# Kernel optimization log

Hardware: AMD Instinct MI355X
Metric: run time of the kernel (lower is better)

The kernel has to match this reference:

```python
import jax, jax.numpy as jnp
import numpy as np
from jax import lax

B, S, T = 256, 128, 64
IN, MID, HID = 4, 128, 512
NH = 4  # attention heads


def setup_inputs() -> dict:
    key = jax.random.key(0)
    ks = iter(jax.random.split(key, 64))
    def p(*shape):
        return jax.random.normal(next(ks), shape, jnp.float32) * 0.05
    d = {}
    d["src"] = jax.random.normal(next(ks), (B, S, IN), jnp.float32)
    d["trg"] = jax.random.normal(next(ks), (B, T, IN), jnp.float32)
    # fc_in: IN -> MID//4 -> MID//2 -> MID
    d["fi_w1"] = p(MID // 4, IN); d["fi_b1"] = p(MID // 4)
    d["fi_w2"] = p(MID // 2, MID // 4); d["fi_b2"] = p(MID // 2)
    d["fi_w3"] = p(MID, MID // 2); d["fi_b3"] = p(MID)
    # encoder: 2-layer bidirectional LSTM (layer0 in=MID, layer1 in=2*HID)
    for name, ind in [("e0", MID), ("e1", 2 * HID)]:
        for sfx in ["f", "b"]:
            d[name + sfx + "_wih"] = p(4 * HID, ind)
            d[name + sfx + "_whh"] = p(4 * HID, HID)
            d[name + sfx + "_bih"] = p(4 * HID)
            d[name + sfx + "_bhh"] = p(4 * HID)
    d["attnfc_w"] = p(MID, 2 * HID); d["attnfc_b"] = p(MID)
    d["inproj_w"] = p(3 * MID, MID); d["inproj_b"] = p(3 * MID)
    d["outproj_w"] = p(MID, MID); d["outproj_b"] = p(MID)
    # decoder: 2-layer unidirectional LSTM (layer0 in=MID, layer1 in=HID)
    for name, ind in [("d0", MID), ("d1", HID)]:
        d[name + "_wih"] = p(4 * HID, ind)
        d[name + "_whh"] = p(4 * HID, HID)
        d[name + "_bih"] = p(4 * HID)
        d[name + "_bhh"] = p(4 * HID)
    # fc_out: HID -> MID//2 -> MID//4 -> IN
    d["fo_w1"] = p(MID // 2, HID); d["fo_b1"] = p(MID // 2)
    d["fo_w2"] = p(MID // 4, MID // 2); d["fo_b2"] = p(MID // 4)
    d["fo_w3"] = p(IN, MID // 4); d["fo_b3"] = p(IN)
    return d


def _gelu(x):
    return jax.nn.gelu(x, approximate=False)  # torch default GELU is exact


def _mlp3(x, w1, b1, w2, b2, w3, b3):
    h = _gelu(x @ w1.T + b1)
    h = _gelu(h @ w2.T + b2)
    return h @ w3.T + b3


def _lstm(x, h0, c0, wih, whh, bih, bhh, reverse=False):
    """PyTorch-semantics LSTM layer. x: (B,T,in) -> (hs (B,T,H), h_T, c_T)."""
    xg = jnp.einsum('bti,gi->btg', x, wih) + (bih + bhh)  # fold input GEMM over time
    def step(carry, xt):
        h, c = carry
        g = xt + h @ whh.T
        i, f, gg, o = jnp.split(g, 4, axis=-1)  # torch gate order: i,f,g,o
        c = jax.nn.sigmoid(f) * c + jax.nn.sigmoid(i) * jnp.tanh(gg)
        h = jax.nn.sigmoid(o) * jnp.tanh(c)
        return (h, c), h
    (h, c), hs = lax.scan(step, (h0, c0), jnp.swapaxes(xg, 0, 1), reverse=reverse)
    return jnp.swapaxes(hs, 0, 1), h, c


def _mha(q_in, kv, inproj_w, inproj_b, outproj_w, outproj_b):
    E = q_in.shape[-1]
    dh = E // NH
    wq, wk, wv = jnp.split(inproj_w, 3, axis=0)
    bq, bk, bv = jnp.split(inproj_b, 3)
    q = q_in @ wq.T + bq
    k = kv @ wk.T + bk
    v = kv @ wv.T + bv
    hd = lambda x: x.reshape(x.shape[0], x.shape[1], NH, dh)
    scores = jnp.einsum('bqhd,bkhd->bhqk', hd(q), hd(k)) * (1.0 / float(np.sqrt(dh)))
    a = jax.nn.softmax(scores, axis=-1)
    o = jnp.einsum('bhqk,bkhd->bqhd', a, hd(v)).reshape(q.shape)
    return o @ outproj_w.T + outproj_b


def reference(src, trg,
              fi_w1, fi_b1, fi_w2, fi_b2, fi_w3, fi_b3,
              e0f_wih, e0f_whh, e0f_bih, e0f_bhh, e0b_wih, e0b_whh, e0b_bih, e0b_bhh,
              e1f_wih, e1f_whh, e1f_bih, e1f_bhh, e1b_wih, e1b_whh, e1b_bih, e1b_bhh,
              attnfc_w, attnfc_b, inproj_w, inproj_b, outproj_w, outproj_b,
              d0_wih, d0_whh, d0_bih, d0_bhh, d1_wih, d1_whh, d1_bih, d1_bhh,
              fo_w1, fo_b1, fo_w2, fo_b2, fo_w3, fo_b3):
    bsz = src.shape[0]
    z = jnp.zeros((bsz, HID), src.dtype)
    enc_embed = _mlp3(src, fi_w1, fi_b1, fi_w2, fi_b2, fi_w3, fi_b3)
    # encoder layer 0 (bidirectional)
    l0f, hf0, cf0 = _lstm(enc_embed, z, z, e0f_wih, e0f_whh, e0f_bih, e0f_bhh)
    l0b, hb0, cb0 = _lstm(enc_embed, z, z, e0b_wih, e0b_whh, e0b_bih, e0b_bhh, reverse=True)
    x1 = jnp.concatenate([l0f, l0b], axis=-1)
    # encoder layer 1 (bidirectional)
    l1f, hf1, cf1 = _lstm(x1, z, z, e1f_wih, e1f_whh, e1f_bih, e1f_bhh)
    l1b, hb1, cb1 = _lstm(x1, z, z, e1b_wih, e1b_whh, e1b_bih, e1b_bhh, reverse=True)
    enc_out = jnp.concatenate([l1f, l1b], axis=-1)  # (B,S,2H)
    # h.view(L,2,B,H).sum(dim=1): sum forward+backward final states per layer
    h_l0, c_l0 = hf0 + hb0, cf0 + cb0
    h_l1, c_l1 = hf1 + hb1, cf1 + cb1
    proj_enc = jnp.tanh(enc_out @ attnfc_w.T + attnfc_b)  # (B,S,MID)
    # teacher_forcing_ratio = 1.0 -> decoder inputs are exactly trg[:, 0:T]
    inp = _mlp3(trg, fi_w1, fi_b1, fi_w2, fi_b2, fi_w3, fi_b3)  # (B,T,MID)
    attn_out = _mha(inp, proj_enc, inproj_w, inproj_b, outproj_w, outproj_b)
    dec_input = inp + attn_out
    d0, _, _ = _lstm(dec_input, h_l0, c_l0, d0_wih, d0_whh, d0_bih, d0_bhh)
    d1, _, _ = _lstm(d0, h_l1, c_l1, d1_wih, d1_whh, d1_bih, d1_bhh)
    delta = _mlp3(d1, fo_w1, fo_b1, fo_w2, fo_b2, fo_w3, fo_b3)
    return trg + delta  # pred_t = trg[:, t-1] + delta_t
```

## Files before the change

### kernel.cpp

```cpp
#include <hip/hip_runtime.h>
#include <cstdint>
#include <cstddef>
#include <cstdio>

typedef __bf16 bf16;
typedef __bf16 bf16x8 __attribute__((ext_vector_type(8)));
typedef __bf16 bf16x4 __attribute__((ext_vector_type(4)));
typedef float f32x4 __attribute__((ext_vector_type(4)));

#define DEVFN __device__ __forceinline__

DEVFN float geluf(float x) { return 0.5f * x * (1.0f + erff(x * 0.70710678118654752f)); }
DEVFN float sigmoidf(float x) { return 1.0f / (1.0f + expf(-x)); }

template <int WGM, int WGN, int ACT, bool RES>
__launch_bounds__(WGM * WGN * 64)
__global__ void gemm_bt(const bf16* __restrict__ A, const bf16* __restrict__ W,
                        const float* __restrict__ bias, const bf16* __restrict__ Rsd,
                        bf16* __restrict__ C, int M, int N, int K) {
  constexpr int BM = WGM * 64, BN = WGN * 64, T = WGM * WGN * 64;
  constexpr int NA = BM * 4 / T, NB = BN * 4 / T;
  __shared__ __align__(16) char ldsA[BM * 64];
  __shared__ __align__(16) char ldsB[BN * 64];
  const int tid = threadIdx.x;
// ... 130 lines not shown
                              int M, int N, int K) {
  constexpr int WGM = 2, WGN = 1;
  constexpr int BM = WGM * 64, BN = WGN * 64, T = WGM * WGN * 64;
  constexpr int NA = BM * 4 / T, NB = BN * 4 / T;
  __shared__ __align__(16) char ldsA[BM * 64];
  __shared__ __align__(16) char ldsB[BN * 64];
  const int tid = threadIdx.x;
  const int lane = tid & 63, wave = tid >> 6;
  const int wm = wave % WGM, wn = wave / WGM;
  const int l16 = lane & 15, quad = lane >> 4;
  const int bm0 = blockIdx.x * BM, bn0 = blockIdx.y * BN;

  f32x4 acc[4][4] = {};
  for (int k0 = 0; k0 < K; k0 += 32) {
    bf16x8 ta[NA], tb[NB];
#pragma unroll
    for (int i = 0; i < NA; ++i) {
      int lin = i * T + tid;
      int row = bm0 + (lin >> 2), seg = lin & 3;
      int t = row >> 8, b = row & 255;
      ta[i] = *(const bf16x8*)(HC + (size_t)t * 131072 + (size_t)((k0 >> 3) + seg) * 2048 + b * 8);
    }
#pragma unroll
    for (int i = 0; i < NB; ++i) {
      int lin = i * T + tid;
      int row = lin >> 2, seg = lin & 3;
      tb[i] = *(const bf16x8*)(W + (size_t)(bn0 + row) * K + k0 + seg * 8);
    }
#pragma unroll
    for (int i = 0; i < NA; ++i) *(bf16x8*)(ldsA + (i * T + tid) * 16) = ta[i];
#pragma unroll
    for (int i = 0; i < NB; ++i) *(bf16x8*)(ldsB + (i * T + tid) * 16) = tb[i];
    __syncthreads();
    bf16x8 af[4], bfrag[4];
#pragma unroll
    for (int mi = 0; mi < 4; ++mi)
      af[mi] = *(const bf16x8*)(ldsA + (wm * 64 + mi * 16 + l16) * 64 + quad * 16);
#pragma unroll
    for (int ni = 0; ni < 4; ++ni)
      bfrag[ni] = *(const bf16x8*)(ldsB + (wn * 64 + ni * 16 + l16) * 64 + quad * 16);
#pragma unroll
    for (int mi = 0; mi < 4; ++mi)
#pragma unroll
      for (int ni = 0; ni < 4; ++ni)
        acc[mi][ni] = __builtin_amdgcn_mfma_f32_16x16x32_bf16(af[mi], bfrag[ni], acc[mi][ni], 0, 0, 0);
    __syncthreads();
  }
#pragma unroll
  for (int mi = 0; mi < 4; ++mi) {
#pragma unroll
    for (int ni = 0; ni < 4; ++ni) {
      int col = bn0 + wn * 64 + ni * 16 + l16;
      float bv = bias[col];
#pragma unroll
      for (int r = 0; r < 4; ++r) {
        int row = bm0 + wm * 64 + mi * 16 + quad * 4 + r;
        float x = geluf(acc[mi][ni][r] + bv);
        C[(size_t)row * N + col] = (bf16)x;
      }
    }
  }
}

template <int HCMODE>
DEVFN void xg_tile(const bf16* __restrict__ A, int tbase, const bf16* __restrict__ W,
                   const float* __restrict__ bias, bf16* __restrict__ C,
                   int K, int bm0, int bn0, int tid, bf16* ldsA, bf16* ldsB) {
  const int lane = tid & 63, wave = tid >> 6;
  const int wm = wave & 1, wn = wave >> 1;
  const int l16 = lane & 15, quad = lane >> 4;
  f32x4 acc[4][4] = {};
  for (int k0 = 0; k0 < K; k0 += 32) {
    bf16x8 ta, tb0, tb1;
    {
      int row = bm0 + (tid >> 2), seg = tid & 3;
      if (HCMODE) {
        int t = tbase + (row >> 8), b = row & 255;
        ta = *(const bf16x8*)(A + (size_t)t * 262144 + (size_t)((k0 >> 3) + seg) * 2048 + b * 8);
      } else {
        ta = *(const bf16x8*)(A + (size_t)row * K + k0 + seg * 8);
      }
    }
    { int row = tid >> 2, seg = tid & 3;
      tb0 = *(const bf16x8*)(W + (size_t)(bn0 + row) * K + k0 + seg * 8); }
    { int lin = 512 + tid; int row = lin >> 2, seg = lin & 3;
      tb1 = *(const bf16x8*)(W + (size_t)(bn0 + row) * K + k0 + seg * 8); }
    *(bf16x8*)(ldsA + tid * 8) = ta;
    *(bf16x8*)(ldsB + tid * 8) = tb0;
    *(bf16x8*)(ldsB + (512 + tid) * 8) = tb1;
    __syncthreads();
    bf16x8 af[4], bfr[4];
#pragma unroll
    for (int mi = 0; mi < 4; ++mi)
      af[mi] = *(const bf16x8*)(ldsA + (wm * 64 + mi * 16 + l16) * 32 + quad * 8);
#pragma unroll
    for (int ni = 0; ni < 4; ++ni)
      bfr[ni] = *(const bf16x8*)(ldsB + (wn * 64 + ni * 16 + l16) * 32 + quad * 8);
#pragma unroll
    for (int mi = 0; mi < 4; ++mi)
#pragma unroll
      for (int ni = 0; ni < 4; ++ni)
        acc[mi][ni] = __builtin_amdgcn_mfma_f32_16x16x32_bf16(af[mi], bfr[ni], acc[mi][ni], 0, 0, 0);
    __syncthreads();
  }
#pragma unroll
  for (int mi = 0; mi < 4; ++mi) {
#pragma unroll
    for (int ni = 0; ni < 4; ++ni) {
      int col = bn0 + wn * 64 + ni * 16 + l16;
      float bv = bias[col];
#pragma unroll
      for (int r = 0; r < 4; ++r) {
        int row = bm0 + wm * 64 + mi * 16 + quad * 4 + r;
        C[(size_t)row * 2048 + col] = (bf16)(acc[mi][ni][r] + bv);
      }
    }
  }
}

struct RDir {
  const bf16* whh_r;
  const bf16* xg;
  bf16* hc;
  int slcOff, rev;
  const bf16* h0;
  float* cbuf;
  bf16* hfin;
};

struct GJob {
  int mode;
  const bf16* Af; const bf16* Ab;
  int tbF, tbB;
  const bf16* Wf; const bf16* Wb;
  const float* bsF; const float* bsB;
  bf16* outF; bf16* outB;
};

__launch_bounds__(512, 1)
__global__ void lstm_rec_g(RDir da, RDir db, int t0, int tc, int Tfull,
                           int* __restrict__ cnts, GJob job) {
  __shared__ __align__(16) char smem[36864];
  const int blk = blockIdx.x;
  const int tid = threadIdx.x;

  if (blk >= 128) {
    if (job.mode == 0) return;
    bf16* ldsA = (bf16*)smem;
    bf16* ldsB = (bf16*)(smem + 8192);
    const int gb = blk - 128;
    const int K = (job.mode == 2) ? 1024 : 128;
    for (int tile = gb; tile < 512; tile += 128) {
      int dir = tile >> 8;
      int rem = tile & 255;
      int mi = rem >> 3, ni = rem & 7;
      const bf16* A = dir ? job.Ab : job.Af;
      int tb = dir ? job.tbB : job.tbF;
      const bf16* W = dir ? job.Wb : job.Wf;
      const float* bs = dir ? job.bsB : job.bsF;
      bf16* C = dir ? job.outB : job.outF;
      if (job.mode == 2)
        xg_tile<1>(A, tb, W, bs, C, K, mi * 128, ni * 256, tid, ldsA, ldsB);
      else
        xg_tile<0>(A, tb, W, bs, C, K, mi * 128, ni * 256, tid, ldsA, ldsB);
    }
    return;
  }

  bf16* whh_lds = (bf16*)smem;
  bf16* hstg = (bf16*)(smem + 32768);
  const RDir d = (blk >= 64) ? db : da;
  const int slice = blk & 63;
  const int colBase = slice * 32, unitBase = slice * 8;
  const int w = tid >> 6, lane = tid & 63;
  const int l16 = lane & 15, quad = lane >> 4;

  for (int e = tid * 8; e < 32 * 512; e += 512 * 8) {
    int c = e >> 9, k0 = e & 511;
    bf16x8 v = *(const bf16x8*)(d.whh_r + (size_t)(colBase + c) * 512 + k0);
    *(bf16x8*)(whh_lds + ((k0 >> 3) << 8) + (c << 3)) = v;
  }
  float cst[2][2];
#pragma unroll
  for (int m = 0; m < 2; ++m)
#pragma unroll
    for (int i = 0; i < 2; ++i) {
      int b = (w * 2 + i) * 16 + l16;
      cst[m][i] = d.cbuf[(size_t)b * 512 + unitBase + m * 4 + quad];
    }
  __syncthreads();

  int* cnt = cnts + (blk & 64);
  const int b0 = (w * 2) * 16 + l16;
  const int b1 = b0 + 16;

  for (int s = 0; s < tc; ++s) {
    const int sg = t0 + s;
    const int t = d.rev ? (Tfull - 1 - sg) : sg;
    const int lt = d.rev ? (tc - 1 - s) : s;

    bf16x4 gxr[2][2];
#pragma unroll
    for (int m = 0; m < 2; ++m)
#pragma unroll
      for (int i = 0; i < 2; ++i) {
        int b = b0 + i * 16;
        gxr[m][i] = *(const bf16x4*)(d.xg + ((size_t)lt * 256 + b) * 2048 + colBase + m * 16 + quad * 4);
      }
    bf16x8 hr[16][2];
    if (sg == 0) {
      const bf16* hp0 = d.h0 + (size_t)b0 * 512 + quad * 8;
      const bf16* hp1 = d.h0 + (size_t)b1 * 512 + quad * 8;
#pragma unroll
      for (int kk = 0; kk < 16; ++kk) {
        hr[kk][0] = *(const bf16x8*)(hp0 + kk * 32);
        hr[kk][1] = *(const bf16x8*)(hp1 + kk * 32);
      }
    } else {
      const int tp = d.rev ? (t + 1) : (t - 1);
      const bf16* hc = d.hc + (size_t)tp * 262144 + (size_t)d.slcOff * 2048;
#pragma unroll
      for (int kk = 0; kk < 16; ++kk) {
        int u8 = kk * 4 + quad;
        hr[kk][0] = *(const bf16x8*)(hc + u8 * 2048 + (size_t)b0 * 8);
        hr[kk][1] = *(const bf16x8*)(hc + u8 * 2048 + (size_t)b1 * 8);
      }
    }
    __builtin_amdgcn_sched_barrier(0);

    f32x4 acc[2][2] = {};
#pragma unroll
    for (int kk = 0; kk < 16; ++kk) {
      bf16x8 a0 = *(const bf16x8*)(whh_lds + kk * 1024 + quad * 256 + l16 * 8);
      bf16x8 a1 = *(const bf16x8*)(whh_lds + kk * 1024 + quad * 256 + 128 + l16 * 8);
      acc[0][0] = __builtin_amdgcn_mfma_f32_16x16x32_bf16(a0, hr[kk][0], acc[0][0], 0, 0, 0);
      acc[1][0] = __builtin_amdgcn_mfma_f32_16x16x32_bf16(a1, hr[kk][0], acc[1][0], 0, 0, 0);
      acc[0][1] = __builtin_amdgcn_mfma_f32_16x16x32_bf16(a0, hr[kk][1], acc[0][1], 0, 0, 0);
      acc[1][1] = __builtin_amdgcn_mfma_f32_16x16x32_bf16(a1, hr[kk][1], acc[1][1], 0, 0, 0);
    }
#pragma unroll
    for (int m = 0; m < 2; ++m)
#pragma unroll
      for (int i = 0; i < 2; ++i) {
        float gi = acc[m][i][0] + (float)gxr[m][i][0];
        float gf = acc[m][i][1] + (float)gxr[m][i][1];
        float gg = acc[m][i][2] + (float)gxr[m][i][2];
        float go = acc[m][i][3] + (float)gxr[m][i][3];
        float cn = sigmoidf(gf) * cst[m][i] + sigmoidf(gi) * tanhf(gg);
        float hv = sigmoidf(go) * tanhf(cn);
        cst[m][i] = cn;
        int b = (w * 2 + i) * 16 + l16;
        hstg[b * 8 + m * 4 + quad] = (bf16)hv;
      }
    __syncthreads();
    {
      unsigned long long v = *(const unsigned long long*)(hstg + tid * 4);
      __hip_atomic_store((unsigned long long*)(d.hc + (size_t)t * 262144 +
                                               (size_t)(d.slcOff + slice) * 2048 + tid * 4),
                         v, __ATOMIC_RELAXED, __HIP_MEMORY_SCOPE_AGENT);
    }
    __syncthreads();
    if (s < tc - 1 && tid == 0)
      __hip_atomic_fetch_add(cnt, 1, __ATOMIC_RELAXED, __HIP_MEMORY_SCOPE_AGENT);
    if (sg == Tfull - 1 && d.hfin && tid < 256) {
      const unsigned long long* p = (const unsigned long long*)(hstg + tid * 8);
      unsigned long long* r2 = (unsigned long long*)(d.hfin + (size_t)tid * 512 + unitBase);
      r2[0] = p[0]; r2[1] = p[1];
    }
    if (s < tc - 1) {
      if (w == 0) {
        int target = 64 * (s + 1), guard = 0;
        while (__hip_atomic_load(cnt, __ATOMIC_RELAXED, __HIP_MEMORY_SCOPE_AGENT) < target) {
          __builtin_amdgcn_s_sleep(2);
          if (++guard > (1 << 22)) break;
        }
      }
      __syncthreads();
    }
  }
#pragma unroll
  for (int m = 0; m < 2; ++m)
#pragma unroll
    for (int i = 0; i < 2; ++i) {
      int b = (w * 2 + i) * 16 + l16;
      d.cbuf[(size_t)b * 512 + unitBase + m * 4 + quad] = cst[m][i];
    }
}

__launch_bounds__(512, 1)
__global__ void lstm_dec_fused(
    const bf16* __restrict__ whh0, const bf16* __restrict__ xg0,
    bf16* __restrict__ hc0, const bf16* __restrict__ h0d0, float* __restrict__ c0buf,
    const bf16* __restrict__ whh1, const bf16* __restrict__ wih1, const float* __restrict__ bias1,
    bf16* __restrict__ hc1, const bf16* __restrict__ h0d1,
    float* __restrict__ c1buf, int* __restrict__ cnts) {
  const int blk = blockIdx.x;
  const int tid = threadIdx.x;
  const int w = tid >> 6, lane = tid & 63;
  const int l16 = lane & 15, quad = lane >> 4;
  constexpr int TC = 64;

  __shared__ __align__(16) bf16 wldsA[32 * 512];
  __shared__ __align__(16) bf16 wldsB[32 * 512];
  __shared__ __align__(16) bf16 hstg[256 * 8];

  int* cnt0 = cnts;
  int* cnt1 = cnts + 64;
  const int b0 = (w * 2) * 16 + l16;
  const int b1 = b0 + 16;

  if (blk < 64) {
    const int slice = blk;
    const int colBase = slice * 32;
    for (int e = tid * 8; e < 32 * 512; e += 512 * 8) {
      int c = e >> 9, k0 = e & 511;
      bf16x8 v = *(const bf16x8*)(whh0 + (size_t)(colBase + c) * 512 + k0);
      *(bf16x8*)(wldsA + ((k0 >> 3) << 8) + (c << 3)) = v;
    }
    float cst[2][2];
#pragma unroll
    for (int m = 0; m < 2; ++m)
#pragma unroll
      for (int i = 0; i < 2; ++i) {
        int b = (w * 2 + i) * 16 + l16;
        cst[m][i] = c0buf[(size_t)b * 512 + slice * 8 + m * 4 + quad];
      }
    __syncthreads();

    for (int s = 0; s < TC; ++s) {
      bf16x4 gxr[2][2];
#pragma unroll
      for (int m = 0; m < 2; ++m)
#pragma unroll
        for (int i = 0; i < 2; ++i) {
          int b = b0 + i * 16;
          gxr[m][i] = *(const bf16x4*)(xg0 + ((size_t)s * 256 + b) * 2048 + colBase + m * 16 + quad * 4);
        }
      bf16x8 hr[16][2];
      if (s == 0) {
        const bf16* hp0 = h0d0 + (size_t)b0 * 512 + quad * 8;
        const bf16* hp1 = h0d0 + (size_t)b1 * 512 + quad * 8;
#pragma unroll
        for (int kk = 0; kk < 16; ++kk) {
          hr[kk][0] = *(const bf16x8*)(hp0 + kk * 32);
          hr[kk][1] = *(const bf16x8*)(hp1 + kk * 32);
        }
      } else {
        const bf16* hc = hc0 + (size_t)(s - 1) * 131072;
#pragma unroll
        for (int kk = 0; kk < 16; ++kk) {
          int u8 = kk * 4 + quad;
          hr[kk][0] = *(const bf16x8*)(hc + u8 * 2048 + (size_t)b0 * 8);
          hr[kk][1] = *(const bf16x8*)(hc + u8 * 2048 + (size_t)b1 * 8);
        }
      }
      __builtin_amdgcn_sched_barrier(0);
      f32x4 acc[2][2] = {};
#pragma unroll
      for (int kk = 0; kk < 16; ++kk) {
        bf16x8 a0 = *(const bf16x8*)(wldsA + kk * 1024 + quad * 256 + l16 * 8);
        bf16x8 a1 = *(const bf16x8*)(wldsA + kk * 1024 + quad * 256 + 128 + l16 * 8);
        acc[0][0] = __builtin_amdgcn_mfma_f32_16x16x32_bf16(a0, hr[kk][0], acc[0][0], 0, 0, 0);
        acc[1][0] = __builtin_amdgcn_mfma_f32_16x16x32_bf16(a1, hr[kk][0], acc[1][0], 0, 0, 0);
        acc[0][1] = __builtin_amdgcn_mfma_f32_16x16x32_bf16(a0, hr[kk][1], acc[0][1], 0, 0, 0);
        acc[1][1] = __builtin_amdgcn_mfma_f32_16x16x32_bf16(a1, hr[kk][1], acc[1][1], 0, 0, 0);
      }
#pragma unroll
      for (int m = 0; m < 2; ++m)
#pragma unroll
        for (int i = 0; i < 2; ++i) {
          float gi = acc[m][i][0] + (float)gxr[m][i][0];
          float gf = acc[m][i][1] + (float)gxr[m][i][1];
          float gg = acc[m][i][2] + (float)gxr[m][i][2];
          float go = acc[m][i][3] + (float)gxr[m][i][3];
          float cn = sigmoidf(gf) * cst[m][i] + sigmoidf(gi) * tanhf(gg);
          float hv = sigmoidf(go) * tanhf(cn);
          cst[m][i] = cn;
          int b = (w * 2 + i) * 16 + l16;
          hstg[b * 8 + m * 4 + quad] = (bf16)hv;
        }
      __syncthreads();
      {
        unsigned long long v = *(const unsigned long long*)(hstg + tid * 4);
        __hip_atomic_store((unsigned long long*)(hc0 + (size_t)s * 131072 + slice * 2048 + tid * 4),
                           v, __ATOMIC_RELAXED, __HIP_MEMORY_SCOPE_AGENT);
      }
      __syncthreads();
      if (tid == 0)
        __hip_atomic_fetch_add(cnt0, 1, __ATOMIC_RELAXED, __HIP_MEMORY_SCOPE_AGENT);
      if (s < TC - 1) {
        if (w == 0) {
          int target = 64 * (s + 1), guard = 0;
          while (__hip_atomic_load(cnt0, __ATOMIC_RELAXED, __HIP_MEMORY_SCOPE_AGENT) < target) {
            __builtin_amdgcn_s_sleep(2);
            if (++guard > (1 << 22)) break;
          }
        }
        __syncthreads();
      }
    }
#pragma unroll
    for (int m = 0; m < 2; ++m)
#pragma unroll
      for (int i = 0; i < 2; ++i) {
        int b = (w * 2 + i) * 16 + l16;
        c0buf[(size_t)b * 512 + slice * 8 + m * 4 + quad] = cst[m][i];
      }
  } else {
    const int slice = blk - 64;
    const int colBase = slice * 32;
    for (int e = tid * 8; e < 32 * 512; e += 512 * 8) {
      int c = e >> 9, k0 = e & 511;
      bf16x8 v = *(const bf16x8*)(whh1 + (size_t)(colBase + c) * 512 + k0);
      *(bf16x8*)(wldsA + ((k0 >> 3) << 8) + (c << 3)) = v;
      bf16x8 u = *(const bf16x8*)(wih1 + (size_t)(colBase + c) * 512 + k0);
      *(bf16x8*)(wldsB + ((k0 >> 3) << 8) + (c << 3)) = u;
    }
    float gbv[2][4];
#pragma unroll
    for (int m = 0; m < 2; ++m)
#pragma unroll
      for (int r = 0; r < 4; ++r) gbv[m][r] = bias1[colBase + m * 16 + quad * 4 + r];
    float cst[2][2];
#pragma unroll
    for (int m = 0; m < 2; ++m)
#pragma unroll
      for (int i = 0; i < 2; ++i) {
        int b = (w * 2 + i) * 16 + l16;
        cst[m][i] = c1buf[(size_t)b * 512 + slice * 8 + m * 4 + quad];
      }
    __syncthreads();
    if (w == 0) {
      int guard = 0;
      while (__hip_atomic_load(cnt0, __ATOMIC_RELAXED, __HIP_MEMORY_SCOPE_AGENT) < 64) {
        __builtin_amdgcn_s_sleep(2);
        if (++guard > (1 << 22)) break;
      }
    }
    __syncthreads();

    for (int s = 0; s < TC; ++s) {
      f32x4 acc[2][2] = {};
      {
        bf16x8 hr[16][2];
        if (s == 0) {
          const bf16* hp0 = h0d1 + (size_t)b0 * 512 + quad * 8;
          const bf16* hp1 = h0d1 + (size_t)b1 * 512 + quad * 8;
#pragma unroll
          for (int kk = 0; kk < 16; ++kk) {
            hr[kk][0] = *(const bf16x8*)(hp0 + kk * 32);
            hr[kk][1] = *(const bf16x8*)(hp1 + kk * 32);
          }
        } else {
          const bf16* hc = hc1 + (size_t)(s - 1) * 131072;
#pragma unroll
          for (int kk = 0; kk < 16; ++kk) {
            int u8 = kk * 4 + quad;
            hr[kk][0] = *(const bf16x8*)(hc + u8 * 2048 + (size_t)b0 * 8);
            hr[kk][1] = *(const bf16x8*)(hc + u8 * 2048 + (size_t)b1 * 8);
          }
        }
        __builtin_amdgcn_sched_barrier(0);
#pragma unroll
        for (int kk = 0; kk < 16; ++kk) {
          bf16x8 a0 = *(const bf16x8*)(wldsA + kk * 1024 + quad * 256 + l16 * 8);
          bf16x8 a1 = *(const bf16x8*)(wldsA + kk * 1024 + quad * 256 + 128 + l16 * 8);
          acc[0][0] = __builtin_amdgcn_mfma_f32_16x16x32_bf16(a0, hr[kk][0], acc[0][0], 0, 0, 0);
          acc[1][0] = __builtin_amdgcn_mfma_f32_16x16x32_bf16(a1, hr[kk][0], acc[1][0], 0, 0, 0);
          acc[0][1] = __builtin_amdgcn_mfma_f32_16x16x32_bf16(a0, hr[kk][1], acc[0][1], 0, 0, 0);
          acc[1][1] = __builtin_amdgcn_mfma_f32_16x16x32_bf16(a1, hr[kk][1], acc[1][1], 0, 0, 0);
        }
      }
      {
        const bf16* xc = hc0 + (size_t)s * 131072;
        bf16x8 xr[16][2];
#pragma unroll
        for (int kk = 0; kk < 16; ++kk) {
          int u8 = kk * 4 + quad;
          xr[kk][0] = *(const bf16x8*)(xc + u8 * 2048 + (size_t)b0 * 8);
          xr[kk][1] = *(const bf16x8*)(xc + u8 * 2048 + (size_t)b1 * 8);
        }
        __builtin_amdgcn_sched_barrier(0);
#pragma unroll
        for (int kk = 0; kk < 16; ++kk) {
          bf16x8 aw0 = *(const bf16x8*)(wldsB + kk * 1024 + quad * 256 + l16 * 8);
          bf16x8 aw1 = *(const bf16x8*)(wldsB + kk * 1024 + quad * 256 + 128 + l16 * 8);
          acc[0][0] = __builtin_amdgcn_mfma_f32_16x16x32_bf16(aw0, xr[kk][0], acc[0][0], 0, 0, 0);
          acc[1][0] = __builtin_amdgcn_mfma_f32_16x16x32_bf16(aw1, xr[kk][0], acc[1][0], 0, 0, 0);
          acc[0][1] = __builtin_amdgcn_mfma_f32_16x16x32_bf16(aw0, xr[kk][1], acc[0][1], 0, 0, 0);
          acc[1][1] = __builtin_amdgcn_mfma_f32_16x16x32_bf16(aw1, xr[kk][1], acc[1][1], 0, 0, 0);
        }
      }
#pragma unroll
      for (int m = 0; m < 2; ++m)
#pragma unroll
        for (int i = 0; i < 2; ++i) {
          float gi = acc[m][i][0] + gbv[m][0];
          float gf = acc[m][i][1] + gbv[m][1];
          float gg = acc[m][i][2] + gbv[m][2];
          float go = acc[m][i][3] + gbv[m][3];
          float cn = sigmoidf(gf) * cst[m][i] + sigmoidf(gi) * tanhf(gg);
          float hv = sigmoidf(go) * tanhf(cn);
          cst[m][i] = cn;
          int b = (w * 2 + i) * 16 + l16;
          hstg[b * 8 + m * 4 + quad] = (bf16)hv;
        }
      __syncthreads();
      {
        unsigned long long v = *(const unsigned long long*)(hstg + tid * 4);
        __hip_atomic_store((unsigned long long*)(hc1 + (size_t)s * 131072 + slice * 2048 + tid * 4),
                           v, __ATOMIC_RELAXED, __HIP_MEMORY_SCOPE_AGENT);
      }
      __syncthreads();
      if (s < TC - 1) {
        if (tid == 0)
          __hip_atomic_fetch_add(cnt1, 1, __ATOMIC_RELAXED, __HIP_MEMORY_SCOPE_AGENT);
        if (w == 0) {
          int t1 = 64 * (s + 1), t0n = 64 * (s + 2), guard = 0;
          while (true) {
            int v1 = __hip_atomic_load(cnt1, __ATOMIC_RELAXED, __HIP_MEMORY_SCOPE_AGENT);
            int v0 = __hip_atomic_load(cnt0, __ATOMIC_RELAXED, __HIP_MEMORY_SCOPE_AGENT);
            if (v1 >= t1 && v0 >= t0n) break;
            __builtin_amdgcn_s_sleep(2);
            if (++guard > (1 << 22)) break;
          }
        }
        __syncthreads();
      }
    }
#pragma unroll
    for (int m = 0; m < 2; ++m)
#pragma unroll
      for (int i = 0; i < 2; ++i) {
        int b = (w * 2 + i) * 16 + l16;
        c1buf[(size_t)b * 512 + slice * 8 + m * 4 + quad] = cst[m][i];
      }
  }
}

__launch_bounds__(256)
__global__ void fc_in_mlp(const float* __restrict__ x, bf16* __restrict__ y, int rows, int tmod,
                          const float* __restrict__ w1, const float* __restrict__ b1,
                          const float* __restrict__ w2, const float* __restrict__ b2,
                          const float* __restrict__ w3, const float* __restrict__ b3) {
  __shared__ float sm[10592];
  const int tid = threadIdx.x;
  for (int i = tid; i < 10592; i += 256) {
    float v;
    if (i < 128) v = w1[i];
    else if (i < 160) v = b1[i - 128];
    else if (i < 2208) v = w2[i - 160];
    else if (i < 2272) v = b2[i - 2208];
    else if (i < 10464) v = w3[i - 2272];
    else v = b3[i - 10464];
    sm[i] = v;
  }
  __syncthreads();
  int row = blockIdx.x * 256 + tid;
  if (row >= rows) return;
  int orow = tmod ? ((row % tmod) * 256 + row / tmod) : row;
  float xin[4];
#pragma unroll
  for (int k = 0; k < 4; ++k) xin[k] = x[(size_t)row * 4 + k];
  float h1[32];
#pragma unroll
  for (int j = 0; j < 32; ++j) {
    float a = sm[128 + j];
#pragma unroll
    for (int k = 0; k < 4; ++k) a += sm[j * 4 + k] * xin[k];
    h1[j] = geluf(a);
  }
  float h2[64];
#pragma unroll
  for (int j = 0; j < 64; ++j) {
    float a = sm[2208 + j];
#pragma unroll
    for (int k = 0; k < 32; ++k) a += sm[160 + j * 32 + k] * h1[k];
    h2[j] = geluf(a);
  }
  for (int c = 0; c < 8; ++c) {
    float accv[16];
#pragma unroll
    for (int j = 0; j < 16; ++j) accv[j] = sm[10464 + c * 16 + j];
#pragma unroll
    for (int j = 0; j < 16; ++j) {
#pragma unroll
      for (int k = 0; k < 64; ++k) accv[j] += sm[2272 + (c * 16 + j) * 64 + k] * h2[k];
    }
#pragma unroll
    for (int j = 0; j < 16; ++j) y[(size_t)orow * 128 + c * 16 + j] = (bf16)accv[j];
  }
}

__launch_bounds__(256)
__global__ void fc_out_tail(const bf16* __restrict__ h1in, const float* __restrict__ trg,
                            float* __restrict__ out, int rows,
                            const float* __restrict__ w2, const float* __restrict__ b2,
                            const float* __restrict__ w3, const float* __restrict__ b3) {
  __shared__ float sm[2212];
  const int tid = threadIdx.x;
  for (int i = tid; i < 2212; i += 256) {
    float v;
    if (i < 2048) v = w2[i];
    else if (i < 2080) v = b2[i - 2048];
    else if (i < 2208) v = w3[i - 2080];
    else v = b3[i - 2208];
    sm[i] = v;
  }
  __syncthreads();
  int row = blockIdx.x * 256 + tid;
  if (row >= rows) return;
  int b = row >> 6, t = row & 63;
  const bf16* h1p = h1in + ((size_t)t * 256 + b) * 64;
  float h1[64];
#pragma unroll
  for (int k = 0; k < 64; ++k) h1[k] = (float)h1p[k];
  float h2[32];
#pragma unroll
  for (int j = 0; j < 32; ++j) {
    float a = sm[2048 + j];
#pragma unroll
    for (int k = 0; k < 64; ++k) a += sm[j * 64 + k] * h1[k];
    h2[j] = geluf(a);
  }
#pragma unroll
  for (int dd = 0; dd < 4; ++dd) {
    float a = sm[2208 + dd];
#pragma unroll
    for (int k = 0; k < 32; ++k) a += sm[2080 + dd * 32 + k] * h2[k];
    out[(size_t)row * 4 + dd] = trg[(size_t)row * 4 + dd] + a;
  }
}

__launch_bounds__(128)
__global__ void attention_kernel(const bf16* __restrict__ Q, const bf16* __restrict__ K,
                                 const bf16* __restrict__ V, bf16* __restrict__ O) {
  __shared__ bf16 qs[64 * 32];
  __shared__ float ks[128 * 33];
  __shared__ bf16 vs[128 * 32];
  __shared__ float sc[64 * 132];
  const int b = blockIdx.x, h = blockIdx.y, tid = threadIdx.x;
  for (int i = tid; i < 64 * 32; i += 128) {
    int t = i >> 5, dd = i & 31;
    qs[i] = Q[((size_t)t * 256 + b) * 128 + h * 32 + dd];
  }
  for (int i = tid; i < 128 * 32; i += 128) {
    int s = i >> 5, dd = i & 31;
    size_t ridx = ((size_t)s * 256 + b) * 128 + h * 32 + dd;
    ks[s * 33 + dd] = (float)K[ridx];
    vs[i] = V[ridx];
  }
  __syncthreads();
  const float scale = 0.17677669529663687f;
  for (int i = tid; i < 64 * 128; i += 128) {
    int t = i >> 7, s = i & 127;
    float a = 0.f;
#pragma unroll
    for (int dd = 0; dd < 32; ++dd) a += (float)qs[t * 32 + dd] * ks[s * 33 + dd];
    sc[t * 132 + s] = a * scale;
  }
  __syncthreads();
  if (tid < 64) {
    float m = -1e30f;
    for (int s = 0; s < 128; ++s) m = fmaxf(m, sc[tid * 132 + s]);
    float sum = 0.f;
    for (int s = 0; s < 128; ++s) { float e = expf(sc[tid * 132 + s] - m); sc[tid * 132 + s] = e; sum += e; }
    float r = 1.0f / sum;
    for (int s = 0; s < 128; ++s) sc[tid * 132 + s] *= r;
  }
  __syncthreads();
  for (int i = tid; i < 64 * 32; i += 128) {
    int t = i >> 5, dd = i & 31;
    float a = 0.f;
    for (int s = 0; s < 128; ++s) a += sc[t * 132 + s] * (float)vs[s * 32 + dd];
    O[((size_t)t * 256 + b) * 128 + h * 32 + dd] = (bf16)a;
  }
}

__global__ void reorder_gate_rows(const float* __restrict__ in, bf16* __restrict__ out, int K) {
  int i = blockIdx.x * 256 + threadIdx.x;
  if (i >= 2048 * K) return;
  int r = i / K, k = i - r * K;
  int nr = 4 * (r & 511) + (r >> 9);
  out[(size_t)nr * K + k] = (bf16)in[i];
}

__global__ void combine_bias(const float* __restrict__ a, const float* __restrict__ b,
                             float* __restrict__ out) {
  int i = blockIdx.x * 256 + threadIdx.x;
  if (i >= 2048) return;
  out[4 * (i & 511) + (i >> 9)] = a[i] + b[i];
}

__global__ void f2b(const float* __restrict__ in, bf16* __restrict__ out, int n) {
  int i = blockIdx.x * 256 + threadIdx.x;
  if (i < n) out[i] = (bf16)in[i];
}

__global__ void zero_u32(uint32_t* __restrict__ p, int n) {
  int i = blockIdx.x * 256 + threadIdx.x;
  if (i < n) p[i] = 0u;
}

__global__ void dec_state_init(const bf16* __restrict__ hf, const bf16* __restrict__ hb,
                               const float* __restrict__ cf, const float* __restrict__ cb,
                               bf16* __restrict__ hout, float* __restrict__ cout) {
  int i = blockIdx.x * 256 + threadIdx.x;
  if (i >= 256 * 512) return;
  hout[i] = (bf16)((float)hf[i] + (float)hb[i]);
  cout[i] = cf[i] + cb[i];
}

extern "C" void kernel_launch(void* const* d_in, const int* in_sizes, int n_in,
                              void* d_out, int out_size, void* d_ws, size_t ws_size,
                              hipStream_t stream) {
  (void)in_sizes; (void)n_in; (void)out_size;
  const float* src = (const float*)d_in[0];
  const float* trg = (const float*)d_in[1];
  const float* fi_w1 = (const float*)d_in[2];
  const float* fi_b1 = (const float*)d_in[3];
  const float* fi_w2 = (const float*)d_in[4];
  const float* fi_b2 = (const float*)d_in[5];
  const float* fi_w3 = (const float*)d_in[6];
  const float* fi_b3 = (const float*)d_in[7];
  const float* wih_in[6] = {(const float*)d_in[8],  (const float*)d_in[12], (const float*)d_in[16],
                            (const float*)d_in[20], (const float*)d_in[30], (const float*)d_in[34]};
  const float* whh_in[6] = {(const float*)d_in[9],  (const float*)d_in[13], (const float*)d_in[17],
                            (const float*)d_in[21], (const float*)d_in[31], (const float*)d_in[35]};
  const float* bih_in[6] = {(const float*)d_in[10], (const float*)d_in[14], (const float*)d_in[18],
                            (const float*)d_in[22], (const float*)d_in[32], (const float*)d_in[36]};
  const float* bhh_in[6] = {(const float*)d_in[11], (const float*)d_in[15], (const float*)d_in[19],
                            (const float*)d_in[23], (const float*)d_in[33], (const float*)d_in[37]};
  const int kin[6] = {128, 128, 1024, 1024, 128, 512};
  const float* attnfc_w = (const float*)d_in[24];
  const float* attnfc_b = (const float*)d_in[25];
  const float* inproj_w = (const float*)d_in[26];
  const float* inproj_b = (const float*)d_in[27];
  const float* outproj_w = (const float*)d_in[28];
  const float* outproj_b = (const float*)d_in[29];
  const float* fo_w1 = (const float*)d_in[38];
  const float* fo_b1 = (const float*)d_in[39];
  const float* fo_w2 = (const float*)d_in[40];
  const float* fo_b2 = (const float*)d_in[41];
  const float* fo_w3 = (const float*)d_in[42];
  const float* fo_b3 = (const float*)d_in[43];
  float* out = (float*)d_out;

  char* base = (char*)d_ws;
  size_t o = 0;
  auto take = [&](size_t bytes) -> char* {
    char* p = base + o;
    o = (o + bytes + 255) & ~(size_t)255;
    return p;
  };
  bf16* wr_wih[6]; for (int i = 0; i < 6; ++i) wr_wih[i] = (bf16*)take((size_t)2048 * kin[i] * 2);
  bf16* wr_whh[6]; for (int i = 0; i < 6; ++i) wr_whh[i] = (bf16*)take((size_t)2048 * 512 * 2);
  float* bias_l[6]; for (int i = 0; i < 6; ++i) bias_l[i] = (float*)take(2048 * 4);
  bf16* attnfc_wb = (bf16*)take((size_t)128 * 1024 * 2);
  bf16* inproj_wb = (bf16*)take((size_t)384 * 128 * 2);
  bf16* outproj_wb = (bf16*)take((size_t)128 * 128 * 2);
  bf16* fo_w1b = (bf16*)take((size_t)64 * 512 * 2);
  bf16* h0_0 = (bf16*)take((size_t)6 * 256 * 512 * 2);
  bf16* hf_0 = (bf16*)take((size_t)6 * 256 * 512 * 2);
  float* c_0 = (float*)take((size_t)6 * 256 * 512 * 4);
  int* flags = (int*)take(4096 * 4);
  bf16* h0_[6]; bf16* hf_[6]; float* c_[6];
  for (int i = 0; i < 6; ++i) {
    h0_[i] = h0_0 + (size_t)i * 256 * 512;
    hf_[i] = hf_0 + (size_t)i * 256 * 512;
    c_[i] = c_0 + (size_t)i * 256 * 512;
  }
  char* RA = take((size_t)64 << 20);
  char* RB = take((size_t)64 << 20);
  char* XG = take((size_t)64 << 20);
  bf16* embed = (bf16*)take((size_t)32768 * 128 * 2);
  size_t required = o;
  if (required > ws_size) {
    fprintf(stderr, "[kernel_launch] ws_size=%zu < required=%zu — aborting launch\n",
            ws_size, required);
    return;
  }

  bf16* x1_hc    = (bf16*)RA;
  bf16* proj_enc = (bf16*)RA;
  bf16* inp      = (bf16*)(RA + ((size_t)8 << 20));
  bf16* qb       = (bf16*)(RA + ((size_t)12 << 20));
  bf16* kb       = (bf16*)(RA + ((size_t)16 << 20));
  bf16* vb       = (bf16*)(RA + ((size_t)24 << 20));
  bf16* attnb    = (bf16*)(RA + ((size_t)32 << 20));
  bf16* dec_in   = (bf16*)(RA + ((size_t)36 << 20));
  bf16* fc1out   = (bf16*)(RA + ((size_t)40 << 20));
  bf16* enc_hc   = (bf16*)RB;
  bf16* hc0      = (bf16*)RB;
  bf16* hc1      = (bf16*)(RB + ((size_t)20 << 20));
  bf16* bufF[2]  = {(bf16*)XG, (bf16*)(XG + ((size_t)32 << 20))};
  bf16* bufB[2]  = {(bf16*)(XG + ((size_t)16 << 20)), (bf16*)(XG + ((size_t)48 << 20))};
  bf16* xg_dec   = (bf16*)XG;

  for (int i = 0; i < 6; ++i) {
    reorder_gate_rows<<<dim3((2048 * kin[i] + 255) / 256), 256, 0, stream>>>(wih_in[i], wr_wih[i], kin[i]);
    reorder_gate_rows<<<dim3(4096), 256, 0, stream>>>(whh_in[i], wr_whh[i], 512);
    combine_bias<<<dim3(8), 256, 0, stream>>>(bih_in[i], bhh_in[i], bias_l[i]);
  }
  f2b<<<dim3(512), 256, 0, stream>>>(attnfc_w, attnfc_wb, 128 * 1024);
  f2b<<<dim3(192), 256, 0, stream>>>(inproj_w, inproj_wb, 384 * 128);
  f2b<<<dim3(64), 256, 0, stream>>>(outproj_w, outproj_wb, 128 * 128);
  f2b<<<dim3(128), 256, 0, stream>>>(fo_w1, fo_w1b, 64 * 512);
  zero_u32<<<dim3(1024), 256, 0, stream>>>((uint32_t*)h0_0, 4 * 256 * 512 / 2);
  zero_u32<<<dim3(2048), 256, 0, stream>>>((uint32_t*)c_0, 4 * 256 * 512);
  zero_u32<<<dim3(16), 256, 0, stream>>>((uint32_t*)flags, 4096);

  fc_in_mlp<<<dim3(128), 256, 0, stream>>>(src, embed, 32768, 128, fi_w1, fi_b1, fi_w2, fi_b2, fi_w3, fi_b3);

  constexpr int TCC = 16, NCH = 8;
  gemm_bt<2, 2, 0, false><<<dim3(32, 16), 256, 0, stream>>>(
      embed, wr_wih[0], bias_l[0], nullptr, bufF[0], 4096, 2048, 128);
  gemm_bt<2, 2, 0, false><<<dim3(32, 16), 256, 0, stream>>>(
      embed + (size_t)(128 - TCC) * 256 * 128, wr_wih[1], bias_l[1], nullptr, bufB[0], 4096, 2048, 128);
  for (int c = 0; c < NCH; ++c) {
    GJob job{};
    if (c < NCH - 1) {
      int n = c + 1;
      job.mode = 1;
      job.Af = embed + (size_t)(TCC * n) * 256 * 128;
      job.Ab = embed + (size_t)(128 - TCC * n - TCC) * 256 * 128;
      job.Wf = wr_wih[0]; job.Wb = wr_wih[1];
      job.bsF = bias_l[0]; job.bsB = bias_l[1];
      job.outF = bufF[n & 1]; job.outB = bufB[n & 1];
    }
    RDir f{wr_whh[0], bufF[c & 1], x1_hc, 0, 0, h0_[0], c_[0], hf_[0]};
    RDir bk{wr_whh[1], bufB[c & 1], x1_hc, 64, 1, h0_[1], c_[1], hf_[1]};
    lstm_rec_g<<<dim3(256), 512, 0, stream>>>(f, bk, c * TCC, TCC, 128, flags + c * 128, job);
  }
  gemm_hcA<2, 2, 0><<<dim3(32, 16), 256, 0, stream>>>(
      x1_hc, 0, wr_wih[2], bias_l[2], bufF[0], 4096, 2048, 1024);
  gemm_hcA<2, 2, 0><<<dim3(32, 16), 256, 0, stream>>>(
      x1_hc, 128 - TCC, wr_wih[3], bias_l[3], bufB[0], 4096, 2048, 1024);
  for (int c = 0; c < NCH; ++c) {
    GJob job{};
    if (c < NCH - 1) {
      int n = c + 1;
      job.mode = 2;
      job.Af = x1_hc; job.Ab = x1_hc;
      job.tbF = TCC * n; job.tbB = 128 - TCC * n - TCC;
      job.Wf = wr_wih[2]; job.Wb = wr_wih[3];
      job.bsF = bias_l[2]; job.bsB = bias_l[3];
      job.outF = bufF[n & 1]; job.outB = bufB[n & 1];
    }
    RDir f{wr_whh[2], bufF[c & 1], enc_hc, 0, 0, h0_[2], c_[2], hf_[2]};
    RDir bk{wr_whh[3], bufB[c & 1], enc_hc, 64, 1, h0_[3], c_[3], hf_[3]};
    lstm_rec_g<<<dim3(256), 512, 0, stream>>>(f, bk, c * TCC, TCC, 128, flags + 1024 + c * 128, job);
  }

  gemm_hcA<2, 2, 1><<<dim3(256, 1), 256, 0, stream>>>(
      enc_hc, 0, attnfc_wb, attnfc_b, proj_enc, 32768, 128, 1024);

  fc_in_mlp<<<dim3(64), 256, 0, stream>>>(trg, inp, 16384, 64, fi_w1, fi_b1, fi_w2, fi_b2, fi_w3, fi_b3);

  gemm_bt<2, 2, 0, false><<<dim3(128, 1), 256, 0, stream>>>(inp, inproj_wb, inproj_b, nullptr, qb, 16384, 128, 128);
  gemm_bt<2, 2, 0, false><<<dim3(256, 1), 256, 0, stream>>>(proj_enc, inproj_wb + (size_t)128 * 128, inproj_b + 128, nullptr, kb, 32768, 128, 128);
  gemm_bt<2, 2, 0, false><<<dim3(256, 1), 256, 0, stream>>>(proj_enc, inproj_wb + (size_t)256 * 128, inproj_b + 256, nullptr, vb, 32768, 128, 128);
  attention_kernel<<<dim3(256, 4), 128, 0, stream>>>(qb, kb, vb, attnb);
  gemm_bt<2, 2, 0, true><<<dim3(128, 1), 256, 0, stream>>>(attnb, outproj_wb, outproj_b, inp, dec_in, 16384, 128, 128);

  dec_state_init<<<dim3(512), 256, 0, stream>>>(hf_[0], hf_[1], c_[0], c_[1], h0_[4], c_[4]);
  dec_state_init<<<dim3(512), 256, 0, stream>>>(hf_[2], hf_[3], c_[2], c_[3], h0_[5], c_[5]);

  gemm_bt<2, 2, 0, false><<<dim3(128, 16), 256, 0, stream>>>(dec_in, wr_wih[4], bias_l[4], nullptr, xg_dec, 16384, 2048, 128);
  lstm_dec_fused<<<dim3(128), 512, 0, stream>>>(
      wr_whh[4], xg_dec, hc0, h0_[4], c_[4],
      wr_whh[5], wr_wih[5], bias_l[5], hc1, h0_[5], c_[5],
      flags + 2048);

  gemm_hc_fcout<<<dim3(128, 1), 128, 0, stream>>>(hc1, fo_w1b, fo_b1, fc1out, 16384, 64, 512);
  fc_out_tail<<<dim3(64), 256, 0, stream>>>(fc1out, trg, out, 16384, fo_w2, fo_b2, fo_w3, fo_b3);
}
```

Baseline: 3.590 ms.

## Split decoder LSTM batch across two blocks per column slice

The fused decoder LSTM kernel now launches 256 blocks instead of 128, and each column slice is split over two blocks that each handle half the batch (128 rows). Each wave then does half the MFMA work and half the h loads per step, which shortens the per-step critical path of the recurrence. Layer 1 also issues its h and x loads together before both MFMA loops rather than in two separate phases. In exchange, twice as many blocks take part in the grid-wide counter barrier, and each block loads its full weight slice into LDS, so weight traffic from global memory doubles.

```diff
diff --git a/kernel.cpp b/kernel.cpp
--- a/kernel.cpp
+++ b/kernel.cpp
@@ -456,87 +456,70 @@
 
   __shared__ __align__(16) bf16 wldsA[32 * 512];
   __shared__ __align__(16) bf16 wldsB[32 * 512];
-  __shared__ __align__(16) bf16 hstg[256 * 8];
+  __shared__ __align__(16) bf16 hstg[128 * 8];
 
   int* cnt0 = cnts;
   int* cnt1 = cnts + 64;
-  const int b0 = (w * 2) * 16 + l16;
-  const int b1 = b0 + 16;
-
-  if (blk < 64) {
-    const int slice = blk;
+
+  if (blk < 128) {
+    const int slice = blk >> 1, bh = blk & 1;
     const int colBase = slice * 32;
+    const int b0 = bh * 128 + w * 16 + l16;
     for (int e = tid * 8; e < 32 * 512; e += 512 * 8) {
       int c = e >> 9, k0 = e & 511;
       bf16x8 v = *(const bf16x8*)(whh0 + (size_t)(colBase + c) * 512 + k0);
       *(bf16x8*)(wldsA + ((k0 >> 3) << 8) + (c << 3)) = v;
     }
-    float cst[2][2];
+    float cst[2];
 #pragma unroll
     for (int m = 0; m < 2; ++m)
-#pragma unroll
-      for (int i = 0; i < 2; ++i) {
-        int b = (w * 2 + i) * 16 + l16;
-        cst[m][i] = c0buf[(size_t)b * 512 + slice * 8 + m * 4 + quad];
-      }
+      cst[m] = c0buf[(size_t)b0 * 512 + slice * 8 + m * 4 + quad];
     __syncthreads();
 
     for (int s = 0; s < TC; ++s) {
-      bf16x4 gxr[2][2];
+      bf16x4 gxr[2];
 #pragma unroll
       for (int m = 0; m < 2; ++m)
-#pragma unroll
-        for (int i = 0; i < 2; ++i) {
-          int b = b0 + i * 16;
-          gxr[m][i] = *(const bf16x4*)(xg0 + ((size_t)s * 256 + b) * 2048 + colBase + m * 16 + quad * 4);
-        }
-      bf16x8 hr[16][2];
+        gxr[m] = *(const bf16x4*)(xg0 + ((size_t)s * 256 + b0) * 2048 + colBase + m * 16 + quad * 4);
+      bf16x8 hr[16];
       if (s == 0) {
-        const bf16* hp0 = h0d0 + (size_t)b0 * 512 + quad * 8;
-        const bf16* hp1 = h0d0 + (size_t)b1 * 512 + quad * 8;
-#pragma unroll
-        for (int kk = 0; kk < 16; ++kk) {
-          hr[kk][0] = *(const bf16x8*)(hp0 + kk * 32);
-          hr[kk][1] = *(const bf16x8*)(hp1 + kk * 32);
-        }
+        const bf16* hp = h0d0 + (size_t)b0 * 512 + quad * 8;
+#pragma unroll
+        for (int kk = 0; kk < 16; ++kk) hr[kk] = *(const bf16x8*)(hp + kk * 32);
       } else {
         const bf16* hc = hc0 + (size_t)(s - 1) * 131072;
 #pragma unroll
         for (int kk = 0; kk < 16; ++kk) {
           int u8 = kk * 4 + quad;
-          hr[kk][0] = *(const bf16x8*)(hc + u8 * 2048 + (size_t)b0 * 8);
-          hr[kk][1] = *(const bf16x8*)(hc + u8 * 2048 + (size_t)b1 * 8);
+          hr[kk] = *(const bf16x8*)(hc + u8 * 2048 + (size_t)b0 * 8);
         }
       }
       __builtin_amdgcn_sched_barrier(0);
-      f32x4 acc[2][2] = {};
+      f32x4 acc[2] = {};
 #pragma unroll
       for (int kk = 0; kk < 16; ++kk) {
         bf16x8 a0 = *(const bf16x8*)(wldsA + kk * 1024 + quad * 256 + l16 * 8);
         bf16x8 a1 = *(const bf16x8*)(wldsA + kk * 1024 + quad * 256 + 128 + l16 * 8);
-        acc[0][0] = __builtin_amdgcn_mfma_f32_16x16x32_bf16(a0, hr[kk][0], acc[0][0], 0, 0, 0);
-        acc[1][0] = __builtin_amdgcn_mfma_f32_16x16x32_bf16(a1, hr[kk][0], acc[1][0], 0, 0, 0);
-        acc[0][1] = __builtin_amdgcn_mfma_f32_16x16x32_bf16(a0, hr[kk][1], acc[0][1], 0, 0, 0);
-        acc[1][1] = __builtin_amdgcn_mfma_f32_16x16x32_bf16(a1, hr[kk][1], acc[1][1], 0, 0, 0);
-      }
-#pragma unroll
-      for (int m = 0; m < 2; ++m)
-#pragma unroll
-        for (int i = 0; i < 2; ++i) {
-          float gi = acc[m][i][0] + (float)gxr[m][i][0];
-          float gf = acc[m][i][1] + (float)gxr[m][i][1];
-          float gg = acc[m][i][2] + (float)gxr[m][i][2];
-          float go = acc[m][i][3] + (float)gxr[m][i][3];
-          float cn = sigmoidf(gf) * cst[m][i] + sigmoidf(gi) * tanhf(gg);
-          float hv = sigmoidf(go) * tanhf(cn);
-          cst[m][i] = cn;
-          int b = (w * 2 + i) * 16 + l16;
-          hstg[b * 8 + m * 4 + quad] = (bf16)hv;
-        }
+        acc[0] = __builtin_amdgcn_mfma_f32_16x16x32_bf16(a0, hr[kk], acc[0], 0, 0, 0);
+        acc[1] = __builtin_amdgcn_mfma_f32_16x16x32_bf16(a1, hr[kk], acc[1], 0, 0, 0);
+      }
+#pragma unroll
+      for (int m = 0; m < 2; ++m) {
+        float gi = acc[m][0] + (float)gxr[m][0];
+        float gf = acc[m][1] + (float)gxr[m][1];
+        float gg = acc[m][2] + (float)gxr[m][2];
+        float go = acc[m][3] + (float)gxr[m][3];
+        float cn = sigmoidf(gf) * cst[m] + sigmoidf(gi) * tanhf(gg);
+        float hv = sigmoidf(go) * tanhf(cn);
+        cst[m] = cn;
+        int lb = w * 16 + l16;
+        hstg[lb * 8 + m * 4 + quad] = (bf16)hv;
+      }
       __syncthreads();
-      {
+      if (tid < 256) {
         unsigned long long v = *(const unsigned long long*)(hstg + tid * 4);
-        __hip_atomic_store((unsigned long long*)(hc0 + (size_t)s * 131072 + slice * 2048 + tid * 4),
+        __hip_atomic_store((unsigned long long*)(hc0 + (size_t)s * 131072 +
+                                                 slice * 2048 + bh * 1024 + tid * 4),
                            v, __ATOMIC_RELAXED, __HIP_MEMORY_SCOPE_AGENT);
       }
       __syncthreads();
@@ -544,7 +527,7 @@
         __hip_atomic_fetch_add(cnt0, 1, __ATOMIC_RELAXED, __HIP_MEMORY_SCOPE_AGENT);
       if (s < TC - 1) {
         if (w == 0) {
-          int target = 64 * (s + 1), guard = 0;
+          int target = 128 * (s + 1), guard = 0;
           while (__hip_atomic_load(cnt0, __ATOMIC_RELAXED, __HIP_MEMORY_SCOPE_AGENT) < target) {
             __builtin_amdgcn_s_sleep(2);
             if (++guard > (1 << 22)) break;
@@ -555,14 +538,11 @@
     }
 #pragma unroll
     for (int m = 0; m < 2; ++m)
-#pragma unroll
-      for (int i = 0; i < 2; ++i) {
-        int b = (w * 2 + i) * 16 + l16;
-        c0buf[(size_t)b * 512 + slice * 8 + m * 4 + quad] = cst[m][i];
-      }
+      c0buf[(size_t)b0 * 512 + slice * 8 + m * 4 + quad] = cst[m];
   } else {
-    const int slice = blk - 64;
+    const int idx = blk - 128, slice = idx >> 1, bh = idx & 1;
     const int colBase = slice * 32;
+    const int b0 = bh * 128 + w * 16 + l16;
     for (int e = tid * 8; e < 32 * 512; e += 512 * 8) {
       int c = e >> 9, k0 = e & 511;
       bf16x8 v = *(const bf16x8*)(whh1 + (size_t)(colBase + c) * 512 + k0);
@@ -575,18 +555,14 @@
     for (int m = 0; m < 2; ++m)
 #pragma unroll
       for (int r = 0; r < 4; ++r) gbv[m][r] = bias1[colBase + m * 16 + quad * 4 + r];
-    float cst[2][2];
+    float cst[2];
 #pragma unroll
     for (int m = 0; m < 2; ++m)
-#pragma unroll
-      for (int i = 0; i < 2; ++i) {
-        int b = (w * 2 + i) * 16 + l16;
-        cst[m][i] = c1buf[(size_t)b * 512 + slice * 8 + m * 4 + quad];
-      }
+      cst[m] = c1buf[(size_t)b0 * 512 + slice * 8 + m * 4 + quad];
     __syncthreads();
     if (w == 0) {
       int guard = 0;
-      while (__hip_atomic_load(cnt0, __ATOMIC_RELAXED, __HIP_MEMORY_SCOPE_AGENT) < 64) {
+      while (__hip_atomic_load(cnt0, __ATOMIC_RELAXED, __HIP_MEMORY_SCOPE_AGENT) < 128) {
         __builtin_amdgcn_s_sleep(2);
         if (++guard > (1 << 22)) break;
       }
@@ -594,75 +570,60 @@
     __syncthreads();
 
     for (int s = 0; s < TC; ++s) {
-      f32x4 acc[2][2] = {};
-      {
-        bf16x8 hr[16][2];
-        if (s == 0) {
-          const bf16* hp0 = h0d1 + (size_t)b0 * 512 + quad * 8;
-          const bf16* hp1 = h0d1 + (size_t)b1 * 512 + quad * 8;
-#pragma unroll
-          for (int kk = 0; kk < 16; ++kk) {
-            hr[kk][0] = *(const bf16x8*)(hp0 + kk * 32);
-            hr[kk][1] = *(const bf16x8*)(hp1 + kk * 32);
-          }
-        } else {
-          const bf16* hc = hc1 + (size_t)(s - 1) * 131072;
-#pragma unroll
-          for (int kk = 0; kk < 16; ++kk) {
-            int u8 = kk * 4 + quad;
-            hr[kk][0] = *(const bf16x8*)(hc + u8 * 2048 + (size_t)b0 * 8);
-            hr[kk][1] = *(const bf16x8*)(hc + u8 * 2048 + (size_t)b1 * 8);
-          }
-        }
-        __builtin_amdgcn_sched_barrier(0);
+      bf16x8 hr[16], xr[16];
+      if (s == 0) {
+        const bf16* hp = h0d1 + (size_t)b0 * 512 + quad * 8;
+#pragma unroll
+        for (int kk = 0; kk < 16; ++kk) hr[kk] = *(const bf16x8*)(hp + kk * 32);
+      } else {
+        const bf16* hc = hc1 + (size_t)(s - 1) * 131072;
 #pragma unroll
         for (int kk = 0; kk < 16; ++kk) {
-          bf16x8 a0 = *(const bf16x8*)(wldsA + kk * 1024 + quad * 256 + l16 * 8);
-          bf16x8 a1 = *(const bf16x8*)(wldsA + kk * 1024 + quad * 256 + 128 + l16 * 8);
-          acc[0][0] = __builtin_amdgcn_mfma_f32_16x16x32_bf16(a0, hr[kk][0], acc[0][0], 0, 0, 0);
-          acc[1][0] = __builtin_amdgcn_mfma_f32_16x16x32_bf16(a1, hr[kk][0], acc[1][0], 0, 0, 0);
-          acc[0][1] = __builtin_amdgcn_mfma_f32_16x16x32_bf16(a0, hr[kk][1], acc[0][1], 0, 0, 0);
-          acc[1][1] = __builtin_amdgcn_mfma_f32_16x16x32_bf16(a1, hr[kk][1], acc[1][1], 0, 0, 0);
+          int u8 = kk * 4 + quad;
+          hr[kk] = *(const bf16x8*)(hc + u8 * 2048 + (size_t)b0 * 8);
         }
       }
       {
         const bf16* xc = hc0 + (size_t)s * 131072;
-        bf16x8 xr[16][2];
 #pragma unroll
         for (int kk = 0; kk < 16; ++kk) {
           int u8 = kk * 4 + quad;
-          xr[kk][0] = *(const bf16x8*)(xc + u8 * 2048 + (size_t)b0 * 8);
-          xr[kk][1] = *(const bf16x8*)(xc + u8 * 2048 + (size_t)b1 * 8);
+          xr[kk] = *(const bf16x8*)(xc + u8 * 2048 + (size_t)b0 * 8);
         }
-        __builtin_amdgcn_sched_barrier(0);
-#pragma unroll
-        for (int kk = 0; kk < 16; ++kk) {
-          bf16x8 aw0 = *(const bf16x8*)(wldsB + kk * 1024 + quad * 256 + l16 * 8);
-          bf16x8 aw1 = *(const bf16x8*)(wldsB + kk * 1024 + quad * 256 + 128 + l16 * 8);
-          acc[0][0] = __builtin_amdgcn_mfma_f32_16x16x32_bf16(aw0, xr[kk][0], acc[0][0], 0, 0, 0);
-          acc[1][0] = __builtin_amdgcn_mfma_f32_16x16x32_bf16(aw1, xr[kk][0], acc[1][0], 0, 0, 0);
-          acc[0][1] = __builtin_amdgcn_mfma_f32_16x16x32_bf16(aw0, xr[kk][1], acc[0][1], 0, 0, 0);
-          acc[1][1] = __builtin_amdgcn_mfma_f32_16x16x32_bf16(aw1, xr[kk][1], acc[1][1], 0, 0, 0);
-        }
-      }
-#pragma unroll
-      for (int m = 0; m < 2; ++m)
-#pragma unroll
-        for (int i = 0; i < 2; ++i) {
-          float gi = acc[m][i][0] + gbv[m][0];
-          float gf = acc[m][i][1] + gbv[m][1];
-          float gg = acc[m][i][2] + gbv[m][2];
-          float go = acc[m][i][3] + gbv[m][3];
-          float cn = sigmoidf(gf) * cst[m][i] + sigmoidf(gi) * tanhf(gg);
-          float hv = sigmoidf(go) * tanhf(cn);
-          cst[m][i] = cn;
-          int b = (w * 2 + i) * 16 + l16;
-          hstg[b * 8 + m * 4 + quad] = (bf16)hv;
-        }
+      }
+      __builtin_amdgcn_sched_barrier(0);
+      f32x4 acc[2] = {};
+#pragma unroll
+      for (int kk = 0; kk < 16; ++kk) {
+        bf16x8 a0 = *(const bf16x8*)(wldsA + kk * 1024 + quad * 256 + l16 * 8);
+        bf16x8 a1 = *(const bf16x8*)(wldsA + kk * 1024 + quad * 256 + 128 + l16 * 8);
+        acc[0] = __builtin_amdgcn_mfma_f32_16x16x32_bf16(a0, hr[kk], acc[0], 0, 0, 0);
+        acc[1] = __builtin_amdgcn_mfma_f32_16x16x32_bf16(a1, hr[kk], acc[1], 0, 0, 0);
+      }
+#pragma unroll
+      for (int kk = 0; kk < 16; ++kk) {
+        bf16x8 aw0 = *(const bf16x8*)(wldsB + kk * 1024 + quad * 256 + l16 * 8);
+        bf16x8 aw1 = *(const bf16x8*)(wldsB + kk * 1024 + quad * 256 + 128 + l16 * 8);
+        acc[0] = __builtin_amdgcn_mfma_f32_16x16x32_bf16(aw0, xr[kk], acc[0], 0, 0, 0);
+        acc[1] = __builtin_amdgcn_mfma_f32_16x16x32_bf16(aw1, xr[kk], acc[1], 0, 0, 0);
+      }
+#pragma unroll
+      for (int m = 0; m < 2; ++m) {
+        float gi = acc[m][0] + gbv[m][0];
+        float gf = acc[m][1] + gbv[m][1];
+        float gg = acc[m][2] + gbv[m][2];
+        float go = acc[m][3] + gbv[m][3];
+        float cn = sigmoidf(gf) * cst[m] + sigmoidf(gi) * tanhf(gg);
+        float hv = sigmoidf(go) * tanhf(cn);
+        cst[m] = cn;
+        int lb = w * 16 + l16;
+        hstg[lb * 8 + m * 4 + quad] = (bf16)hv;
+      }
       __syncthreads();
-      {
+      if (tid < 256) {
         unsigned long long v = *(const unsigned long long*)(hstg + tid * 4);
-        __hip_atomic_store((unsigned long long*)(hc1 + (size_t)s * 131072 + slice * 2048 + tid * 4),
+        __hip_atomic_store((unsigned long long*)(hc1 + (size_t)s * 131072 +
+                                                 slice * 2048 + bh * 1024 + tid * 4),
                            v, __ATOMIC_RELAXED, __HIP_MEMORY_SCOPE_AGENT);
       }
       __syncthreads();
@@ -670,7 +631,7 @@
         if (tid == 0)
           __hip_atomic_fetch_add(cnt1, 1, __ATOMIC_RELAXED, __HIP_MEMORY_SCOPE_AGENT);
         if (w == 0) {
-          int t1 = 64 * (s + 1), t0n = 64 * (s + 2), guard = 0;
+          int t1 = 128 * (s + 1), t0n = 128 * (s + 2), guard = 0;
           while (true) {
             int v1 = __hip_atomic_load(cnt1, __ATOMIC_RELAXED, __HIP_MEMORY_SCOPE_AGENT);
             int v0 = __hip_atomic_load(cnt0, __ATOMIC_RELAXED, __HIP_MEMORY_SCOPE_AGENT);
@@ -684,11 +645,7 @@
     }
 #pragma unroll
     for (int m = 0; m < 2; ++m)
-#pragma unroll
-      for (int i = 0; i < 2; ++i) {
-        int b = (w * 2 + i) * 16 + l16;
-        c1buf[(size_t)b * 512 + slice * 8 + m * 4 + quad] = cst[m][i];
-      }
+      c1buf[(size_t)b0 * 512 + slice * 8 + m * 4 + quad] = cst[m];
   }
 }
 
@@ -1021,7 +978,7 @@
   dec_state_init<<<dim3(512), 256, 0, stream>>>(hf_[2], hf_[3], c_[2], c_[3], h0_[5], c_[5]);
 
   gemm_bt<2, 2, 0, false><<<dim3(128, 16), 256, 0, stream>>>(dec_in, wr_wih[4], bias_l[4], nullptr, xg_dec, 16384, 2048, 128);
-  lstm_dec_fused<<<dim3(128), 512, 0, stream>>>(
+  lstm_dec_fused<<<dim3(256), 512, 0, stream>>>(
       wr_whh[4], xg_dec, hc0, h0_[4], c_[4],
       wr_whh[5], wr_wih[5], bias_l[5], hc1, h0_[5], c_[5],
       flags + 2048);
```

After: 3.055 ms. 1.17x faster.
